# Kernel optimization log

Measured on AMD Instinct MI355X. Metric: run time of the kernel, lower is better.

Reference implementation:

```python
import jax, jax.numpy as jnp
import numpy as np
from jax import lax

NCP = 9  # 3x3 control grid

def _control_points():
    s = int(np.sqrt(NCP))
    pts = np.zeros((NCP, 2), np.float32)
    for i in range(NCP):
        pts[i, 0] = (i % s) / (s - 1) * 2 - 1
        pts[i, 1] = (i // s) / (s - 1) * 2 - 1
    return jnp.asarray(pts)

def _tps_L():
    cp = _control_points()
    d = cp[:, None, :] - cp[None, :, :]
    r2 = (d ** 2).sum(-1)
    r2s = jnp.where(r2 > 0, r2, 1.0)
    K = jnp.where(r2 > 0, r2s * jnp.log(r2s), 0.0)          # [9,9]
    P = jnp.concatenate([jnp.ones((NCP, 1)), cp], axis=1)   # [9,3]
    top = jnp.concatenate([K, P], axis=1)                   # [9,12]
    bot = jnp.concatenate([P.T, jnp.zeros((3, 3))], axis=1) # [3,12]
    return jnp.concatenate([top, bot], axis=0)              # [12,12]

def _conv(x, w, b):
    y = lax.conv_general_dilated(x, w, (1, 1), 'SAME',
                                 dimension_numbers=('NCHW', 'OIHW', 'NCHW'))
    return y + b[None, :, None, None]

def _maxpool2(x):
    return lax.reduce_window(x, -jnp.inf, lax.max, (1, 1, 2, 2), (1, 1, 2, 2), 'VALID')

def _grid_sample(img, grid):
    # bilinear, align_corners=True, zeros padding. img [B,C,H,W], grid [B,H,W,2]
    B, C, H, W = img.shape
    x = (grid[..., 0] + 1.0) * 0.5 * (W - 1)
    y = (grid[..., 1] + 1.0) * 0.5 * (H - 1)
    x0 = jnp.floor(x); y0 = jnp.floor(y)
    wx = x - x0; wy = y - y0
    def gather(ix, iy):
        valid = (ix >= 0) & (ix < W) & (iy >= 0) & (iy < H)
        ixc = jnp.clip(ix, 0, W - 1).astype(jnp.int32)
        iyc = jnp.clip(iy, 0, H - 1).astype(jnp.int32)
        v = jax.vmap(lambda im, yy, xx: im[:, yy, xx])(img, iyc, ixc)  # [B,C,Hg,Wg]
        return v * valid[:, None, :, :].astype(img.dtype)
    v00 = gather(x0, y0); v10 = gather(x0 + 1, y0)
    v01 = gather(x0, y0 + 1); v11 = gather(x0 + 1, y0 + 1)
    w00 = ((1 - wx) * (1 - wy))[:, None]; w10 = (wx * (1 - wy))[:, None]
    w01 = ((1 - wx) * wy)[:, None];       w11 = (wx * wy)[:, None]
    return v00 * w00 + v10 * w10 + v01 * w01 + v11 * w11

def setup_inputs() -> dict:
    key = jax.random.key(0)
    ks = jax.random.split(key, 9)
    B, C, H, W = 32, 1, 256, 256
    x = jax.random.normal(ks[0], (B, C, H, W), jnp.float32)
    def he(k, shape, fan_in):
        return jax.random.normal(k, shape, jnp.float32) * np.sqrt(2.0 / fan_in)
    return {
        'x': x,
        'conv1_w': he(ks[1], (32, 1, 3, 3), 1 * 9),   'conv1_b': jnp.zeros((32,)),
        'conv2_w': he(ks[2], (64, 32, 3, 3), 32 * 9), 'conv2_b': jnp.zeros((64,)),
        'fc1_w': he(ks[3], (256, 1024), 1024),        'fc1_b': jnp.zeros((256,)),
        'fc2_w': he(ks[4], (18, 256), 256) * 0.01,    'fc2_b': jnp.zeros((18,)),
    }

def reference(x, conv1_w, conv1_b, conv2_w, conv2_b, fc1_w, fc1_b, fc2_w, fc2_b):
    B, C, H, W = x.shape
    cp = _control_points()
    L = _tps_L()
    # localization network
    f = jax.nn.relu(_maxpool2(_conv(x, conv1_w, conv1_b)))
    f = jax.nn.relu(_maxpool2(_conv(f, conv2_w, conv2_b)))
    # adaptive avg pool to 4x4 (divisible case)
    Bh, Ch, Hh, Wh = f.shape
    f = f.reshape(Bh, Ch, 4, Hh // 4, 4, Wh // 4).mean(axis=(3, 5))
    f = f.reshape(B, -1)
    h = jax.nn.relu(f @ fc1_w.T + fc1_b)
    disp = (h @ fc2_w.T + fc2_b).reshape(B, NCP, 2)
    target = cp[None] + disp                                  # [B,9,2]
    # batched 12x12 TPS solve
    Y = jnp.concatenate([target, jnp.zeros((B, 3, 2))], axis=1)  # [B,12,2]
    Wfull = jnp.linalg.solve(jnp.broadcast_to(L, (B, 12, 12)), Y)
    Wc, A = Wfull[:, :NCP], Wfull[:, NCP:]                    # [B,9,2], [B,3,2]
    # identity sampling grid (align_corners=True)
    xs = jnp.linspace(-1.0, 1.0, W)
    ys = jnp.linspace(-1.0, 1.0, H)
    gx, gy = jnp.meshgrid(xs, ys)                             # [H,W]
    pts = jnp.stack([gx, gy], axis=-1).reshape(1, H * W, 2)   # [1,N,2]
    # RBF warp
    diffs = pts[:, :, None, :] - cp[None, None, :, :]         # [1,N,9,2]
    r2 = (diffs ** 2).sum(-1)                                 # [1,N,9]
    r2s = jnp.where(r2 > 0, r2, 1.0)
    U = jnp.where(r2 > 0, r2s * jnp.log(r2s), 0.0)            # [1,N,9]
    warp = jnp.einsum('xnk,bkd->bnd', U, Wc)                  # [B,N,2]
    affine = A[:, 0:1] + A[:, 1:2] * pts[..., 0:1] + A[:, 2:3] * pts[..., 1:2]
    wgrid = (affine + warp).reshape(B, H, W, 2)
    return _grid_sample(x, wgrid)
```

## Files before the change

### kernel.cpp

```cpp
#include <hip/hip_runtime.h>
#include <hip/hip_bf16.h>
#include <math.h>

#define BATCH 32
#define IMG 256
#define NCP 9
#define F1P 130

typedef __attribute__((ext_vector_type(8))) short bf16x8;
typedef __attribute__((ext_vector_type(4))) float f32x4;
typedef __attribute__((ext_vector_type(4))) unsigned int uint4v;

__device__ __constant__ float d_cpx[9] = {-1.f,0.f,1.f,-1.f,0.f,1.f,-1.f,0.f,1.f};
__device__ __constant__ float d_cpy[9] = {-1.f,-1.f,-1.f,0.f,0.f,0.f,1.f,1.f,1.f};

__device__ inline unsigned int pack2bf(float a, float b) {
    __hip_bfloat16 ha = __float2bfloat16(a), hb = __float2bfloat16(b);
    unsigned short ua = *(unsigned short*)&ha, ub = *(unsigned short*)&hb;
    return ((unsigned int)ub << 16) | ua;
}

__global__ __launch_bounds__(256) void k_conv1p(const float* __restrict__ x,
        const float* __restrict__ w, const float* __restrict__ bias,
        __hip_bfloat16* __restrict__ f1, const float* __restrict__ w2c,
        __hip_bfloat16* __restrict__ wt, float* __restrict__ linv) {
    int blk = blockIdx.x;
    if (blk >= 2048) {
        int pblk = blk - 2048;
        if (pblk == 0) {
            int j = threadIdx.x;
            if (j >= 24) return;
            const float cx[9] = {-1,0,1,-1,0,1,-1,0,1};
            const float cy[9] = {-1,-1,-1,0,0,0,1,1,1};
            float col[12];
            #pragma unroll
            for (int i = 0; i < 12; ++i) {
                float v;
                if (j < 12) {
                    if (i < 9 && j < 9) {
                        float dx = cx[i] - cx[j], dy = cy[i] - cy[j];
                        float r2 = dx * dx + dy * dy;
                        v = (r2 > 0.f) ? r2 * logf(r2) : 0.f;
                    } else if (i < 9) {
                        v = (j == 9) ? 1.f : ((j == 10) ? cx[i] : cy[i]);
                    } else if (j < 9) {
                        v = (i == 9) ? 1.f : ((i == 10) ? cx[j] : cy[j]);
                    } else v = 0.f;
                } else v = (i == j - 12) ? 1.f : 0.f;
                col[i] = v;
            }
            #pragma unroll
            for (int c = 0; c < 12; ++c) {
                float f[12];
                #pragma unroll
                for (int i = 0; i < 12; ++i) f[i] = __shfl(col[i], c);
                int p = c; float best = fabsf(f[c]);
                #pragma unroll
                for (int r = 0; r < 12; ++r) if (r > c) {
                    float a = fabsf(f[r]);
                    bool g = a > best;
                    best = g ? a : best;
                    p = g ? r : p;
                }
                float oldc = col[c], colp = col[c];
                #pragma unroll
                for (int r = 0; r < 12; ++r) colp = (r == p) ? col[r] : colp;
                #pragma unroll
                for (int r = 0; r < 12; ++r) col[r] = (r == p) ? oldc : col[r];
                col[c] = colp;
                float oldfc = f[c], fpv = f[c];
                #pragma unroll
                for (int r = 0; r < 12; ++r) fpv = (r == p) ? f[r] : fpv;
                #pragma unroll
                for (int r = 0; r < 12; ++r) f[r] = (r == p) ? oldfc : f[r];
                f[c] = fpv;
                float inv = 1.0f / f[c];
                col[c] *= inv;
                #pragma unroll
                for (int r = 0; r < 12; ++r) if (r != c) col[r] = fmaf(-f[r], col[c], col[r]);
            }
            if (j >= 12) {
                #pragma unroll
                for (int i = 0; i < 12; ++i) linv[i * 12 + (j - 12)] = col[i];
            }
            return;
        }
        int t = (pblk - 1) * 256 + threadIdx.x;
        if (t < 18432) {
            int pos = t / 2048, rem = t % 2048, oc = rem >> 5, ic = rem & 31;
            wt[t] = __float2bfloat16(w2c[(oc * 32 + ic) * 9 + pos]);
            return;
        }
        int u = t - 18432;
        if (u < 32 * 2064) {
            int b = u / 2064, q = u % 2064;
            int row, px, ch;
            if (q < 520)       { row = 0;   px = q >> 2;         ch = q & 3; }
            else if (q < 1040) { row = 129; px = (q - 520) >> 2; ch = q & 3; }
            else { int z = q - 1040; row = 1 + (z >> 3); int tt = z & 7;
                   px = (tt < 4) ? 0 : 129; ch = tt & 3; }
            uint4v zero = {0, 0, 0, 0};
            size_t eo = ((((size_t)b * F1P + row) * F1P + px) * 32 + ch * 8);
            *(uint4v*)((char*)f1 + eo * 2) = zero;
        }
        return;
    }
    int tj = blk & 7, ti = (blk >> 3) & 7, b = blk >> 6;
    __shared__ float tile[34 * 34];
    __shared__ float wl[32 * 9];
    __shared__ float bl[32];
    int tid = threadIdx.x;
    for (int i = tid; i < 32 * 9; i += 256) wl[i] = w[i];
    if (tid < 32) bl[tid] = bias[tid];
    const float* xb = x + (size_t)b * IMG * IMG;
    int oy0 = ti * 32 - 1, ox0 = tj * 32 - 1;
    for (int i = tid; i < 34 * 34; i += 256) {
        int yy = i / 34, xx = i % 34;
        int r = oy0 + yy, c = ox0 + xx;
        float v = 0.f;
        if (r >= 0 && r < IMG && c >= 0 && c < IMG) v = xb[r * IMG + c];
        tile[i] = v;
    }
    __syncthreads();
    int oy = tid >> 4, ox = tid & 15;
    float p[16];
    #pragma unroll
    for (int yy = 0; yy < 4; ++yy)
        #pragma unroll
        for (int xx = 0; xx < 4; ++xx)
            p[yy * 4 + xx] = tile[(2 * oy + yy) * 34 + (2 * ox + xx)];
    int gy = ti * 16 + oy, gx = tj * 16 + ox;
    unsigned int u[16];
    #pragma unroll
    for (int oc2 = 0; oc2 < 16; ++oc2) {
        float vv[2];
        #pragma unroll
        for (int h = 0; h < 2; ++h) {
            int oc = oc2 * 2 + h;
            float ww[9];
            #pragma unroll
            for (int k = 0; k < 9; ++k) ww[k] = wl[oc * 9 + k];
            float m = -INFINITY;
            #pragma unroll
            for (int dy = 0; dy < 2; ++dy)
                #pragma unroll
                for (int dx = 0; dx < 2; ++dx) {
                    float s = 0.f;
                    #pragma unroll
                    for (int ky = 0; ky < 3; ++ky)
                        #pragma unroll
                        for (int kx = 0; kx < 3; ++kx)
                            s = fmaf(p[(dy + ky) * 4 + dx + kx], ww[ky * 3 + kx], s);
                    m = fmaxf(m, s);
                }
            vv[h] = fmaxf(m + bl[oc], 0.f);
        }
        u[oc2] = pack2bf(vv[0], vv[1]);
    }
    size_t eo = (((size_t)b * F1P + (gy + 1)) * F1P + (gx + 1)) * 32;
    uint4v* dst = (uint4v*)((char*)f1 + eo * 2);
    #pragma unroll
    for (int q = 0; q < 4; ++q) {
        uint4v vq = { u[q*4+0], u[q*4+1], u[q*4+2], u[q*4+3] };
        dst[q] = vq;
    }
}

__global__ __launch_bounds__(256, 2) void k_conv2m(const __hip_bfloat16* __restrict__ f1,
        const __hip_bfloat16* __restrict__ wt, const float* __restrict__ bias,
        float* __restrict__ feat) {
    __shared__ float red[4][64];
    int tid = threadIdx.x;
    int w = tid >> 6, l = tid & 63;
    int lr = l & 15, lg = l >> 4;
    int blk = blockIdx.x;
    int region = blk & 15;
    int b = blk >> 4;
    int ry = region >> 2, rx = region & 3;
    const __hip_bfloat16* f1b = f1 + (size_t)b * F1P * F1P * 32;

    bf16x8 Bf[4][9];
    #pragma unroll
    for (int n = 0; n < 4; ++n)
        #pragma unroll
        for (int p = 0; p < 9; ++p)
            Bf[n][p] = *(const bf16x8*)(wt + ((size_t)(p * 64 + n * 16 + lr) * 32 + lg * 8));
    float biasv[4];
    #pragma unroll
    for (int n = 0; n < 4; ++n) biasv[n] = bias[n * 16 + lr];

    float fsum[4] = {0.f, 0.f, 0.f, 0.f};

    #pragma unroll 1
    for (int b4 = 0; b4 < 4; ++b4) {
        int pr = b4 * 4 + w;
        int row0 = ry * 32 + 2 * pr;
        #pragma unroll
        for (int xt = 0; xt < 2; ++xt) {
            int x0 = rx * 32 + xt * 16 + lr;
            bf16x8 Af[4][3];
            #pragma unroll
            for (int rr = 0; rr < 4; ++rr)
                #pragma unroll
                for (int dx = 0; dx < 3; ++dx)
                    Af[rr][dx] = *(const bf16x8*)(f1b + ((size_t)(row0 + rr) * F1P + x0 + dx) * 32 + lg * 8);
            #pragma unroll
            for (int n = 0; n < 4; ++n) {
                f32x4 a0 = {0.f, 0.f, 0.f, 0.f}, a1 = {0.f, 0.f, 0.f, 0.f};
                #pragma unroll
                for (int dy = 0; dy < 3; ++dy)
                    #pragma unroll
                    for (int dx = 0; dx < 3; ++dx) {
                        a0 = __builtin_amdgcn_mfma_f32_16x16x32_bf16(Af[dy][dx],     Bf[n][dy * 3 + dx], a0, 0, 0, 0);
                        a1 = __builtin_amdgcn_mfma_f32_16x16x32_bf16(Af[dy + 1][dx], Bf[n][dy * 3 + dx], a1, 0, 0, 0);
                    }
                float p0 = fmaxf(fmaxf(a0[0], a0[1]), fmaxf(a1[0], a1[1]));
                float p1 = fmaxf(fmaxf(a0[2], a0[3]), fmaxf(a1[2], a1[3]));
                fsum[n] += fmaxf(p0 + biasv[n], 0.f) + fmaxf(p1 + biasv[n], 0.f);
            }
        }
    }

    #pragma unroll
    for (int n = 0; n < 4; ++n) {
        fsum[n] += __shfl_xor(fsum[n], 16);
        fsum[n] += __shfl_xor(fsum[n], 32);
    }
    if (l < 16) {
        #pragma unroll
        for (int n = 0; n < 4; ++n) red[w][n * 16 + l] = fsum[n];
    }
    __syncthreads();
    if (tid < 64) {
        float s = red[0][tid] + red[1][tid] + red[2][tid] + red[3][tid];
        feat[(size_t)b * 1024 + tid * 16 + region] = s * (1.0f / 256.0f);
    }
}

__global__ __launch_bounds__(256) void k_fc1(const float* __restrict__ feat,
        const float* __restrict__ w, const float* __restrict__ bias,
        float* __restrict__ h) {
    int wave = threadIdx.x >> 6, lane = threadIdx.x & 63;
    int o = blockIdx.x * 4 + wave;
    int b = o >> 8, j = o & 255;
    const float4* wr = (const float4*)(w + (size_t)j * 1024);
    const float4* fb = (const float4*)(feat + (size_t)b * 1024);
    float s = 0.f;
    #pragma unroll
    for (int i = 0; i < 4; ++i) {
        float4 a = wr[lane + i * 64];
        float4 c = fb[lane + i * 64];
        s = fmaf(a.x, c.x, s); s = fmaf(a.y, c.y, s);
        s = fmaf(a.z, c.z, s); s = fmaf(a.w, c.w, s);
    }
    #pragma unroll
    for (int off = 32; off; off >>= 1) s += __shfl_xor(s, off);
    if (lane == 0) h[o] = fmaxf(s + bias[j], 0.f);
}

__global__ __launch_bounds__(64) void k_head(const float* __restrict__ h,
        const float* __restrict__ w2, const float* __restrict__ b2,
        const float* __restrict__ linv, float* __restrict__ wfull) {
    int b = blockIdx.x;
    int t = threadIdx.x;
    __shared__ float Y[12][2];
    __shared__ float L[144];
    const float* hb = h + (size_t)b * 256;
    for (int i = t; i < 144; i += 64) L[i] = linv[i];
    if (t < 18) {
        const float* wr = w2 + (size_t)t * 256;
        float s = 0.f;
        for (int k = 0; k < 256; ++k) s = fmaf(wr[k], hb[k], s);
        s += b2[t];
        int kk = t >> 1, d = t & 1;
        float cp = (d == 0) ? d_cpx[kk] : d_cpy[kk];
        Y[kk][d] = cp + s;
    }
    if (t >= 18 && t < 24) Y[9 + ((t - 18) >> 1)][(t - 18) & 1] = 0.f;
    __syncthreads();
    if (t < 24) {
        int i = t >> 1, d = t & 1;
        float s = 0.f;
        #pragma unroll
        for (int k = 0; k < 12; ++k) s = fmaf(L[i * 12 + k], Y[k][d], s);
        wfull[b * 24 + i * 2 + d] = s;
    }
}

__global__ __launch_bounds__(256) void k_sample(const float* __restrict__ x,
        const float* __restrict__ wfull, float* __restrict__ out) {
    int py = blockIdx.x & 255;
    int bg = blockIdx.x >> 8;
    int px = threadIdx.x;
    __shared__ float Wf[8][24];
    if (threadIdx.x < 192) {
        int bi = threadIdx.x / 24, q = threadIdx.x % 24;
        Wf[bi][q] = wfull[(bg * 8 + bi) * 24 + q];
    }
    __syncthreads();
    float gx = px * (2.0f / 255.0f) - 1.0f;
    float gy = py * (2.0f / 255.0f) - 1.0f;
    float U[9];
    #pragma unroll
    for (int k = 0; k < 9; ++k) {
        float dx = gx - d_cpx[k], dy = gy - d_cpy[k];
        float r2 = dx * dx + dy * dy;
        U[k] = (r2 > 0.f) ? r2 * logf(r2) : 0.f;
    }
    #pragma unroll
    for (int bi = 0; bi < 8; ++bi) {
        int b = bg * 8 + bi;
        float sx = Wf[bi][18] + Wf[bi][20] * gx + Wf[bi][22] * gy;
        float sy = Wf[bi][19] + Wf[bi][21] * gx + Wf[bi][23] * gy;
        #pragma unroll
        for (int k = 0; k < 9; ++k) {
            sx = fmaf(U[k], Wf[bi][k * 2 + 0], sx);
            sy = fmaf(U[k], Wf[bi][k * 2 + 1], sy);
        }
        float xp = (sx + 1.0f) * 0.5f * 255.0f;
        float yp = (sy + 1.0f) * 0.5f * 255.0f;
        float x0f = floorf(xp), y0f = floorf(yp);
        float wx = xp - x0f, wy = yp - y0f;
        int x0 = (int)x0f, y0 = (int)y0f;
        const float* xb = x + (size_t)b * IMG * IMG;
        float v00, v10, v01, v11;
        {
            int ix, iy; bool valid; int ixc, iyc;
            ix = x0;     iy = y0;
            valid = (ix >= 0) && (ix < IMG) && (iy >= 0) && (iy < IMG);
            ixc = min(max(ix, 0), IMG - 1); iyc = min(max(iy, 0), IMG - 1);
            v00 = valid ? xb[iyc * IMG + ixc] : 0.f;
            ix = x0 + 1; iy = y0;
            valid = (ix >= 0) && (ix < IMG) && (iy >= 0) && (iy < IMG);
            ixc = min(max(ix, 0), IMG - 1); iyc = min(max(iy, 0), IMG - 1);
            v10 = valid ? xb[iyc * IMG + ixc] : 0.f;
            ix = x0;     iy = y0 + 1;
            valid = (ix >= 0) && (ix < IMG) && (iy >= 0) && (iy < IMG);
            ixc = min(max(ix, 0), IMG - 1); iyc = min(max(iy, 0), IMG - 1);
            v01 = valid ? xb[iyc * IMG + ixc] : 0.f;
            ix = x0 + 1; iy = y0 + 1;
            valid = (ix >= 0) && (ix < IMG) && (iy >= 0) && (iy < IMG);
            ixc = min(max(ix, 0), IMG - 1); iyc = min(max(iy, 0), IMG - 1);
            v11 = valid ? xb[iyc * IMG + ixc] : 0.f;
        }
        float r = v00 * (1.f - wx) * (1.f - wy) + v10 * wx * (1.f - wy)
                + v01 * (1.f - wx) * wy        + v11 * wx * wy;
        out[(size_t)b * IMG * IMG + py * IMG + px] = r;
    }
}

extern "C" void kernel_launch(void* const* d_in, const int* in_sizes, int n_in,
                              void* d_out, int out_size, void* d_ws, size_t ws_size,
                              hipStream_t stream) {
    const float* x   = (const float*)d_in[0];
    const float* c1w = (const float*)d_in[1];
    const float* c1b = (const float*)d_in[2];
    const float* c2w = (const float*)d_in[3];
    const float* c2b = (const float*)d_in[4];
    const float* w1  = (const float*)d_in[5];
    const float* b1  = (const float*)d_in[6];
    const float* w2  = (const float*)d_in[7];
    const float* b2  = (const float*)d_in[8];
    float* out = (float*)d_out;

    __hip_bfloat16* f1 = (__hip_bfloat16*)d_ws;
    __hip_bfloat16* wt = f1 + (size_t)32 * F1P * F1P * 32;
    float* fbase = (float*)(wt + 18432);
    float* feat  = fbase;
    float* hbuf  = feat + 32768;
    float* wfull = hbuf + 8192;
    float* linv  = wfull + 768;

    k_conv1p<<<2048 + 331, 256, 0, stream>>>(x, c1w, c1b, f1, c2w, wt, linv);
    k_conv2m<<<BATCH * 16, 256, 0, stream>>>(f1, wt, c2b, feat);
    k_fc1   <<<2048, 256, 0, stream>>>(feat, w1, b1, hbuf);
    k_head  <<<BATCH, 64, 0, stream>>>(hbuf, w2, b2, linv, wfull);
    k_sample<<<1024, 256, 0, stream>>>(x, wfull, out);
}
```

Measured before the change: 67.78 us.

## Fuse TPS head solve into sampler and batch four images per fc1 wave

The k_head launch is removed. Each k_sample block now recomputes the fc2 projection and the 12x12 TPS weight multiply for its 8 images in a prologue. fc1 now has each wave compute one output neuron for four batch images at once, so each weight row is loaded once per four images, and the grid shrinks to 512 blocks. This saves a kernel launch and weight traffic, at the cost of redundant fc2 work: every one of the 256 row-blocks per image group repeats a 256-length dot product per thread, which lengthens the sampler's startup.

```diff
diff --git a/kernel.cpp b/kernel.cpp
--- a/kernel.cpp
+++ b/kernel.cpp
@@ -242,60 +242,80 @@
         float* __restrict__ h) {
     int wave = threadIdx.x >> 6, lane = threadIdx.x & 63;
     int o = blockIdx.x * 4 + wave;
-    int b = o >> 8, j = o & 255;
+    int j = o & 255, g = o >> 8;
     const float4* wr = (const float4*)(w + (size_t)j * 1024);
-    const float4* fb = (const float4*)(feat + (size_t)b * 1024);
-    float s = 0.f;
+    const float4* fb0 = (const float4*)(feat + (size_t)(g * 4 + 0) * 1024);
+    const float4* fb1 = (const float4*)(feat + (size_t)(g * 4 + 1) * 1024);
+    const float4* fb2 = (const float4*)(feat + (size_t)(g * 4 + 2) * 1024);
+    const float4* fb3 = (const float4*)(feat + (size_t)(g * 4 + 3) * 1024);
+    float s0 = 0.f, s1 = 0.f, s2 = 0.f, s3 = 0.f;
     #pragma unroll
     for (int i = 0; i < 4; ++i) {
         float4 a = wr[lane + i * 64];
-        float4 c = fb[lane + i * 64];
-        s = fmaf(a.x, c.x, s); s = fmaf(a.y, c.y, s);
-        s = fmaf(a.z, c.z, s); s = fmaf(a.w, c.w, s);
-    }
-    #pragma unroll
-    for (int off = 32; off; off >>= 1) s += __shfl_xor(s, off);
-    if (lane == 0) h[o] = fmaxf(s + bias[j], 0.f);
-}
-
-__global__ __launch_bounds__(64) void k_head(const float* __restrict__ h,
-        const float* __restrict__ w2, const float* __restrict__ b2,
-        const float* __restrict__ linv, float* __restrict__ wfull) {
-    int b = blockIdx.x;
-    int t = threadIdx.x;
-    __shared__ float Y[12][2];
-    __shared__ float L[144];
-    const float* hb = h + (size_t)b * 256;
-    for (int i = t; i < 144; i += 64) L[i] = linv[i];
-    if (t < 18) {
-        const float* wr = w2 + (size_t)t * 256;
-        float s = 0.f;
-        for (int k = 0; k < 256; ++k) s = fmaf(wr[k], hb[k], s);
-        s += b2[t];
-        int kk = t >> 1, d = t & 1;
-        float cp = (d == 0) ? d_cpx[kk] : d_cpy[kk];
-        Y[kk][d] = cp + s;
-    }
-    if (t >= 18 && t < 24) Y[9 + ((t - 18) >> 1)][(t - 18) & 1] = 0.f;
-    __syncthreads();
-    if (t < 24) {
-        int i = t >> 1, d = t & 1;
-        float s = 0.f;
-        #pragma unroll
-        for (int k = 0; k < 12; ++k) s = fmaf(L[i * 12 + k], Y[k][d], s);
-        wfull[b * 24 + i * 2 + d] = s;
+        float4 c0 = fb0[lane + i * 64];
+        float4 c1 = fb1[lane + i * 64];
+        float4 c2 = fb2[lane + i * 64];
+        float4 c3 = fb3[lane + i * 64];
+        s0 = fmaf(a.x, c0.x, s0); s0 = fmaf(a.y, c0.y, s0);
+        s0 = fmaf(a.z, c0.z, s0); s0 = fmaf(a.w, c0.w, s0);
+        s1 = fmaf(a.x, c1.x, s1); s1 = fmaf(a.y, c1.y, s1);
+        s1 = fmaf(a.z, c1.z, s1); s1 = fmaf(a.w, c1.w, s1);
+        s2 = fmaf(a.x, c2.x, s2); s2 = fmaf(a.y, c2.y, s2);
+        s2 = fmaf(a.z, c2.z, s2); s2 = fmaf(a.w, c2.w, s2);
+        s3 = fmaf(a.x, c3.x, s3); s3 = fmaf(a.y, c3.y, s3);
+        s3 = fmaf(a.z, c3.z, s3); s3 = fmaf(a.w, c3.w, s3);
+    }
+    #pragma unroll
+    for (int off = 32; off; off >>= 1) {
+        s0 += __shfl_xor(s0, off);
+        s1 += __shfl_xor(s1, off);
+        s2 += __shfl_xor(s2, off);
+        s3 += __shfl_xor(s3, off);
+    }
+    if (lane == 0) {
+        float bj = bias[j];
+        h[(size_t)(g * 4 + 0) * 256 + j] = fmaxf(s0 + bj, 0.f);
+        h[(size_t)(g * 4 + 1) * 256 + j] = fmaxf(s1 + bj, 0.f);
+        h[(size_t)(g * 4 + 2) * 256 + j] = fmaxf(s2 + bj, 0.f);
+        h[(size_t)(g * 4 + 3) * 256 + j] = fmaxf(s3 + bj, 0.f);
     }
 }
 
 __global__ __launch_bounds__(256) void k_sample(const float* __restrict__ x,
-        const float* __restrict__ wfull, float* __restrict__ out) {
+        const float* __restrict__ h, const float* __restrict__ w2,
+        const float* __restrict__ b2, const float* __restrict__ linv,
+        float* __restrict__ out) {
     int py = blockIdx.x & 255;
     int bg = blockIdx.x >> 8;
     int px = threadIdx.x;
+    int t = threadIdx.x;
     __shared__ float Wf[8][24];
-    if (threadIdx.x < 192) {
-        int bi = threadIdx.x / 24, q = threadIdx.x % 24;
-        Wf[bi][q] = wfull[(bg * 8 + bi) * 24 + q];
+    __shared__ float Ys[8][24];
+    __shared__ float Lm[144];
+    if (t < 144) Lm[t] = linv[t];
+    if (t < 144) {
+        int bi = t / 18, j = t - bi * 18;
+        const float* hb = h + (size_t)(bg * 8 + bi) * 256;
+        const float* wr = w2 + (size_t)j * 256;
+        float s = 0.f;
+        for (int k = 0; k < 256; ++k) s = fmaf(wr[k], hb[k], s);
+        s += b2[j];
+        int kk = j >> 1, d = j & 1;
+        float cp = (d == 0) ? d_cpx[kk] : d_cpy[kk];
+        Ys[bi][j] = cp + s;
+    }
+    if (t >= 144 && t < 192) {
+        int z = t - 144;
+        Ys[z / 6][18 + z % 6] = 0.f;
+    }
+    __syncthreads();
+    if (t < 192) {
+        int bi = t / 24, q = t - bi * 24;
+        int i = q >> 1, d = q & 1;
+        float s = 0.f;
+        #pragma unroll
+        for (int k = 0; k < 12; ++k) s = fmaf(Lm[i * 12 + k], Ys[bi][k * 2 + d], s);
+        Wf[bi][q] = s;
     }
     __syncthreads();
     float gx = px * (2.0f / 255.0f) - 1.0f;
@@ -368,12 +388,10 @@
     float* fbase = (float*)(wt + 18432);
     float* feat  = fbase;
     float* hbuf  = feat + 32768;
-    float* wfull = hbuf + 8192;
-    float* linv  = wfull + 768;
+    float* linv  = hbuf + 8192;
 
     k_conv1p<<<2048 + 331, 256, 0, stream>>>(x, c1w, c1b, f1, c2w, wt, linv);
     k_conv2m<<<BATCH * 16, 256, 0, stream>>>(f1, wt, c2b, feat);
-    k_fc1   <<<2048, 256, 0, stream>>>(feat, w1, b1, hbuf);
-    k_head  <<<BATCH, 64, 0, stream>>>(hbuf, w2, b2, linv, wfull);
-    k_sample<<<1024, 256, 0, stream>>>(x, wfull, out);
-}
+    k_fc1   <<<512, 256, 0, stream>>>(feat, w1, b1, hbuf);
+    k_sample<<<1024, 256, 0, stream>>>(x, hbuf, w2, b2, linv, out);
+}
```

Result: slower. 82.09 us (+21.1%).
